# Kernel optimization log

Hardware: AMD Instinct MI355X
Metric: run time of the kernel (lower is better)

Reference implementation:

```python
import jax, jax.numpy as jnp
import numpy as np

N = 100_000   # nodes
E = 3_200_000 # edges (avg degree 32)
IN, HID, OUT = 1433, 16, 7  # hardcoded in Method_GCN_Class.__init__


def setup_inputs() -> dict:
    key = jax.random.key(0)
    ks = jax.random.split(key, 6)
    x = jax.random.normal(ks[0], (N, IN), dtype=jnp.float32)
    adj_row = jax.random.randint(ks[1], (E,), 0, N, dtype=jnp.int32)
    adj_col = jax.random.randint(ks[2], (E,), 0, N, dtype=jnp.int32)
    adj_val = jax.random.uniform(ks[3], (E,), dtype=jnp.float32)
    W1 = jax.random.uniform(ks[4], (IN, HID), dtype=jnp.float32)  # nn.init.uniform_
    b1 = jnp.zeros((HID,), dtype=jnp.float32)
    W2 = jax.random.uniform(ks[5], (HID, OUT), dtype=jnp.float32)
    b2 = jnp.zeros((OUT,), dtype=jnp.float32)
    return dict(x=x, adj_row=adj_row, adj_col=adj_col, adj_val=adj_val,
                W1=W1, b1=b1, W2=W2, b2=b2)


def _spmm(row, col, val, dense):
    # torch.sparse.mm(adj, dense) with adj in COO form: out[r] += val*dense[c]
    return jax.ops.segment_sum(val[:, None] * dense[col], row, num_segments=N)


def reference(x, adj_row, adj_col, adj_val, W1, b1, W2, b2):
    # layer 1: graph_conv -> relu (dropout p=0.1 is a no-op at inference)
    h = _spmm(adj_row, adj_col, adj_val, x @ W1) + b1
    h = jax.nn.relu(h)
    # layer 2: graph_conv -> log_softmax over classes
    h = _spmm(adj_row, adj_col, adj_val, h @ W2) + b2
    return jax.nn.log_softmax(h, axis=1)
```

## Files before the change

kernel.cpp:

```cpp
#include <hip/hip_runtime.h>
#include <math.h>

#define IN_F 1433
#define HID  16
#define OUTC 7
#define SCAN_T 1024

#define K1_THREADS 512
#define K1_ROWS_W  8
#define K1_ROWS_B  64
#define KA         768
#define LDSW       17
#define K1_LDS_FLOATS (KA * LDSW)

#define RPB      128
#define BCAP     4480
#define PCH      2048
#define OVF_CAP  131072

typedef float f4_t __attribute__((ext_vector_type(4)));
typedef f4_t uf4 __attribute__((aligned(4)));

__host__ __device__ __forceinline__ int imin(int a, int b) { return a < b ? a : b; }

__global__ __launch_bounds__(256) void zero_i32(int4* __restrict__ p, int n4)
{
    int i = blockIdx.x * blockDim.x + threadIdx.x;
    if (i < n4) p[i] = make_int4(0, 0, 0, 0);
}

__device__ __forceinline__ void k1_body(
    const float* __restrict__ x, const float* __restrict__ W1,
    float* __restrict__ XW, int N, int vbid, float* sW)
{
    const int wave = threadIdx.x >> 6;
    const int lane = threadIdx.x & 63;
    const int ks   = lane & 15;
    const int j4   = lane >> 4;
    const int row0 = vbid * K1_ROWS_B + wave * K1_ROWS_W;

    int xoff[K1_ROWS_W];
#pragma unroll
    for (int r = 0; r < K1_ROWS_W; ++r) {
        int row = row0 + r;
        if (row > N - 1) row = N - 1;
        if (row < 0) row = 0;
        xoff[r] = row * IN_F;
    }

    float acc[K1_ROWS_W][4];
#pragma unroll
    for (int r = 0; r < K1_ROWS_W; ++r)
#pragma unroll
        for (int jj = 0; jj < 4; ++jj) acc[r][jj] = 0.f;

#pragma unroll 1
    for (int p = 0; p < 2; ++p) {
        const int pbase = p ? KA : 0;
        const int pk    = p ? (IN_F - KA) : KA;
        if (p) __syncthreads();
        for (int f = threadIdx.x; f < pk * HID; f += K1_THREADS)
            sW[(f >> 4) * LDSW + (f & 15)] = W1[pbase * HID + f];
        __syncthreads();

        const int nfull = pk >> 6;
#pragma unroll 1
        for (int c = 0; c < nfull; ++c) {
            const int kb = c * 64 + ks * 4;
            uf4 xq[K1_ROWS_W];
#pragma unroll
            for (int r = 0; r < K1_ROWS_W; ++r)
                xq[r] = *(const uf4*)(x + (size_t)xoff[r] + pbase + kb);
            float w[4][4];
#pragma unroll
            for (int kk = 0; kk < 4; ++kk) {
                const float* wr = sW + (size_t)(kb + kk) * LDSW + j4 * 4;
                w[kk][0] = wr[0]; w[kk][1] = wr[1];
                w[kk][2] = wr[2]; w[kk][3] = wr[3];
            }
#pragma unroll
            for (int kk = 0; kk < 4; ++kk)
#pragma unroll
                for (int r = 0; r < K1_ROWS_W; ++r) {
                    const float xv = xq[r][kk];
                    acc[r][0] += xv * w[kk][0];
                    acc[r][1] += xv * w[kk][1];
                    acc[r][2] += xv * w[kk][2];
                    acc[r][3] += xv * w[kk][3];
                }
        }

        const int tb = nfull * 64 + ks * 4;
        if (tb < pk + 3 && (pk & 63)) {
#pragma unroll
            for (int kk = 0; kk < 4; ++kk) {
                const int kloc = tb + kk;
                const bool ok = (kloc < pk);
                const float* wr = sW + (size_t)kloc * LDSW + j4 * 4;
                float w0 = wr[0], w1 = wr[1], w2 = wr[2], w3 = wr[3];
#pragma unroll
                for (int r = 0; r < K1_ROWS_W; ++r) {
                    const float xv = ok ? x[(size_t)xoff[r] + pbase + kloc] : 0.f;
                    acc[r][0] += xv * w0;
                    acc[r][1] += xv * w1;
                    acc[r][2] += xv * w2;
                    acc[r][3] += xv * w3;
                }
            }
        }
    }

#pragma unroll
    for (int m = 1; m <= 8; m <<= 1)
#pragma unroll
        for (int r = 0; r < K1_ROWS_W; ++r)
#pragma unroll
            for (int jj = 0; jj < 4; ++jj)
                acc[r][jj] += __shfl_xor(acc[r][jj], m);

    if (ks == 0) {
#pragma unroll
        for (int r = 0; r < K1_ROWS_W; ++r) {
            const int row = row0 + r;
            if (row >= 0 && row < N) {
                float4 o = make_float4(acc[r][0], acc[r][1], acc[r][2], acc[r][3]);
                *(float4*)(XW + (size_t)row * HID + j4 * 4) = o;
            }
        }
    }
}

__device__ __forceinline__ void partition_body(
    const int* __restrict__ arow, const int* __restrict__ acol,
    const float* __restrict__ aval, int* __restrict__ cursor,
    int2* __restrict__ buckets, int* __restrict__ ovf, int* __restrict__ ovfc,
    int E, int nbuk, int sb, int nsb, int* hist)
{
    const int nch = (E + PCH - 1) / PCH;
    for (int ch = sb; ch < nch; ch += nsb) {
        const int e0 = ch * PCH;
        const int e1 = imin(e0 + PCH, E);
        for (int b = threadIdx.x; b < nbuk; b += K1_THREADS) hist[b] = 0;
        __syncthreads();

        int rr[4], cc[4]; float vv[4];
        int nl = 0;
        const int base = e0 + threadIdx.x * 4;
        if (base + 3 < e1) {
            int4 r4 = *(const int4*)(arow + base);
            int4 c4 = *(const int4*)(acol + base);
            float4 v4 = *(const float4*)(aval + base);
            rr[0]=r4.x; rr[1]=r4.y; rr[2]=r4.z; rr[3]=r4.w;
            cc[0]=c4.x; cc[1]=c4.y; cc[2]=c4.z; cc[3]=c4.w;
            vv[0]=v4.x; vv[1]=v4.y; vv[2]=v4.z; vv[3]=v4.w;
            nl = 4;
        } else {
            for (int i = base; i < e1 && nl < 4; ++i) {
                rr[nl] = arow[i]; cc[nl] = acol[i]; vv[nl] = aval[i];
                ++nl;
            }
        }
        for (int u = 0; u < nl; ++u) atomicAdd(&hist[rr[u] >> 7], 1);
        __syncthreads();

        for (int b = threadIdx.x; b < nbuk; b += K1_THREADS) {
            const int h = hist[b];
            hist[b] = (h > 0) ? atomicAdd(&cursor[b], h) : 0;
        }
        __syncthreads();

        for (int u = 0; u < nl; ++u) {
            const int b = rr[u] >> 7;
            const int pos = atomicAdd(&hist[b], 1);
            if (pos < BCAP) {
                buckets[(size_t)b * BCAP + pos] =
                    make_int2(((rr[u] & (RPB - 1)) << 17) | cc[u],
                              __float_as_int(vv[u]));
            } else {
                int op = atomicAdd(ovfc, 1);
                if (op < OVF_CAP) {
                    ovf[3 * op]     = rr[u];
                    ovf[3 * op + 1] = cc[u];
                    ovf[3 * op + 2] = __float_as_int(vv[u]);
                }
            }
        }
        __syncthreads();
    }
}

__global__ __launch_bounds__(K1_THREADS) void k1_partition(
    const float* __restrict__ x, const float* __restrict__ W1,
    float* __restrict__ XW, int N, int k1b,
    const int* __restrict__ arow, const int* __restrict__ acol,
    const float* __restrict__ aval, int* __restrict__ cursor,
    int2* __restrict__ buckets, int* __restrict__ ovf, int* __restrict__ ovfc,
    int E, int nbuk, int scb)
{
    __shared__ float sW[K1_LDS_FLOATS];
    const int bid = blockIdx.x;
    if ((bid % 4 == 3) && (bid / 4 < scb)) {
        partition_body(arow, acol, aval, cursor, buckets, ovf, ovfc,
                       E, nbuk, bid / 4, scb, (int*)sW);
        return;
    }
    const int k1_idx = bid - imin((bid + 1) / 4, scb);
    if (k1_idx >= k1b) return;
    k1_body(x, W1, XW, N, k1_idx, sW);
}

__global__ __launch_bounds__(512) void bucket_repack(
    const int* __restrict__ cursor, int2* __restrict__ buckets,
    int* __restrict__ rowptrB, int* __restrict__ ovf, int* __restrict__ ovfc,
    int nbuk)
{
    __shared__ int2 ebuf[BCAP];
    __shared__ int rcnt[RPB];
    __shared__ int rcur[RPB];
    __shared__ int rbase[RPB + 1];
    const int b = blockIdx.x;
    const int cnt_b = imin(cursor[b], BCAP);
    int2* src = buckets + (size_t)b * BCAP;

    for (int r = threadIdx.x; r < RPB; r += 512) { rcnt[r] = 0; rcur[r] = 0; }
    __syncthreads();

    for (int i = threadIdx.x; i < cnt_b; i += 512)
        atomicAdd(&rcnt[src[i].x >> 17], 1);
    __syncthreads();

    if (threadIdx.x == 0) {
        int run = 0;
        for (int r = 0; r < RPB; ++r) {
            rbase[r] = run;
            run += (rcnt[r] + 1) & ~1;
        }
        rbase[RPB] = run;
    }
    __syncthreads();

    for (int r = threadIdx.x; r < RPB; r += 512) {
        if (rcnt[r] & 1) {
            const int pp = rbase[r] + rcnt[r];
            if (pp < BCAP) ebuf[pp] = make_int2(0, 0);
        }
    }
    __syncthreads();

    for (int i = threadIdx.x; i < cnt_b; i += 512) {
        const int2 ed = src[i];
        const int rl = ed.x >> 17;
        const int pos = rbase[rl] + atomicAdd(&rcur[rl], 1);
        if (pos < BCAP) {
            ebuf[pos] = make_int2(ed.x & 0x1FFFF, ed.y);
        } else {
            int op = atomicAdd(ovfc, 1);
            if (op < OVF_CAP) {
                ovf[3 * op]     = b * RPB + rl;
                ovf[3 * op + 1] = ed.x & 0x1FFFF;
                ovf[3 * op + 2] = ed.y;
            }
        }
    }
    __syncthreads();

    const int total = imin(rbase[RPB], BCAP);
    for (int i = threadIdx.x; i < total; i += 512) src[i] = ebuf[i];
    for (int r = threadIdx.x; r < RPB; r += 512)
        rowptrB[b * (RPB + 1) + r] = imin(rbase[r], BCAP);
    if (threadIdx.x == 0)
        rowptrB[b * (RPB + 1) + RPB] = total;
}

__global__ __launch_bounds__(256) void ovf_apply16(
    const int* __restrict__ ovf, const int* __restrict__ ovfc,
    const float* __restrict__ XW, float* __restrict__ Hx)
{
    const int n = imin(ovfc[0], OVF_CAP);
    const int tid = blockIdx.x * blockDim.x + threadIdx.x;
    const int stride = gridDim.x * blockDim.x;
    for (int i = tid; i < n; i += stride) {
        const int r = ovf[3 * i], c = ovf[3 * i + 1];
        const float v = __int_as_float(ovf[3 * i + 2]);
        const float* src = XW + (size_t)c * HID;
        float* dst = Hx + (size_t)r * HID;
#pragma unroll
        for (int j = 0; j < HID; ++j) atomicAdd(dst + j, v * src[j]);
    }
}

__global__ __launch_bounds__(256) void ovf_apply7(
    const int* __restrict__ ovf, const int* __restrict__ ovfc,
    const float* __restrict__ h2, float* __restrict__ Ox)
{
    const int n = imin(ovfc[0], OVF_CAP);
    const int tid = blockIdx.x * blockDim.x + threadIdx.x;
    const int stride = gridDim.x * blockDim.x;
    for (int i = tid; i < n; i += stride) {
        const int r = ovf[3 * i], c = ovf[3 * i + 1];
        const float v = __int_as_float(ovf[3 * i + 2]);
        const float* src = h2 + (size_t)c * 8;
        float* dst = Ox + (size_t)r * 8;
#pragma unroll
        for (int j = 0; j < OUTC; ++j) atomicAdd(dst + j, v * src[j]);
    }
}

__global__ __launch_bounds__(256) void spmm16B(
    const int* __restrict__ rowptrB, const int2* __restrict__ buckets,
    const float* __restrict__ XW, const float* __restrict__ Hx,
    const float* __restrict__ b1, const float* __restrict__ W2,
    float* __restrict__ h2, int N)
{
    const int gw = (int)((blockIdx.x * (size_t)blockDim.x + threadIdx.x) >> 6);
    if (gw >= N) return;
    const int lane = threadIdx.x & 63;
    const int j = lane & 15;
    const int w = lane >> 4;
    const int b  = gw >> 7;
    const int rl = gw & (RPB - 1);
    const int rs = rowptrB[b * (RPB + 1) + rl];
    const int re = rowptrB[b * (RPB + 1) + rl + 1];
    const int2* base = buckets + (size_t)b * BCAP;

    float acc = 0.f;
    int k = rs + w * 4;
    while (k + 4 <= re) {
        const int4* q = (const int4*)(base + k);
        int4 A = q[0], B = q[1];
        acc += __int_as_float(A.y) * XW[(size_t)A.x * HID + j];
        acc += __int_as_float(A.w) * XW[(size_t)A.z * HID + j];
        acc += __int_as_float(B.y) * XW[(size_t)B.x * HID + j];
        acc += __int_as_float(B.w) * XW[(size_t)B.z * HID + j];
        k += 16;
    }
    for (; k < re; ++k) {
        int2 a = base[k];
        acc += __int_as_float(a.y) * XW[(size_t)a.x * HID + j];
    }
    acc += __shfl_xor(acc, 16);
    acc += __shfl_xor(acc, 32);
    acc += Hx[(size_t)gw * HID + j];

    const float h = fmaxf(acc + b1[j], 0.f);
    float p[OUTC];
#pragma unroll
    for (int c = 0; c < OUTC; ++c) p[c] = h * W2[j * OUTC + c];
#pragma unroll
    for (int m = 1; m <= 8; m <<= 1)
#pragma unroll
        for (int c = 0; c < OUTC; ++c) p[c] += __shfl_xor(p[c], m);

    if (lane < 8) {
        float o = p[0];
        o = (lane == 1) ? p[1] : o;
        o = (lane == 2) ? p[2] : o;
        o = (lane == 3) ? p[3] : o;
        o = (lane == 4) ? p[4] : o;
        o = (lane == 5) ? p[5] : o;
        o = (lane == 6) ? p[6] : o;
        if (lane == 7) o = 0.f;
        h2[(size_t)gw * 8 + lane] = o;
    }
}

__global__ __launch_bounds__(256) void spmm7B(
    const int* __restrict__ rowptrB, const int2* __restrict__ buckets,
    const float* __restrict__ h2, const float* __restrict__ Ox,
    const float* __restrict__ b2, float* __restrict__ out, int N)
{
    const int gw = (int)((blockIdx.x * (size_t)blockDim.x + threadIdx.x) >> 6);
    if (gw >= N) return;
    const int lane = threadIdx.x & 63;
    const int j = lane & 7;
    const int w = lane >> 3;
    const int b  = gw >> 7;
    const int rl = gw & (RPB - 1);
    const int rs = rowptrB[b * (RPB + 1) + rl];
    const int re = rowptrB[b * (RPB + 1) + rl + 1];
    const int2* base = buckets + (size_t)b * BCAP;

    float acc = 0.f;
    int k = rs + w * 4;
    while (k + 4 <= re) {
        const int4* q = (const int4*)(base + k);
        int4 A = q[0], B = q[1];
        acc += __int_as_float(A.y) * h2[(size_t)A.x * 8 + j];
        acc += __int_as_float(A.w) * h2[(size_t)A.z * 8 + j];
        acc += __int_as_float(B.y) * h2[(size_t)B.x * 8 + j];
        acc += __int_as_float(B.w) * h2[(size_t)B.z * 8 + j];
        k += 32;
    }
    for (; k < re; ++k) {
        int2 a = base[k];
        acc += __int_as_float(a.y) * h2[(size_t)a.x * 8 + j];
    }
    acc += __shfl_xor(acc, 8);
    acc += __shfl_xor(acc, 16);
    acc += __shfl_xor(acc, 32);
    acc += Ox[(size_t)gw * 8 + j];

    const float bias = b2[(j < OUTC) ? j : 0];
    const float val  = acc + bias;
    float mx = (j < OUTC) ? val : -INFINITY;
    mx = fmaxf(mx, __shfl_xor(mx, 1));
    mx = fmaxf(mx, __shfl_xor(mx, 2));
    mx = fmaxf(mx, __shfl_xor(mx, 4));
    float ex = (j < OUTC) ? expf(val - mx) : 0.f;
    ex += __shfl_xor(ex, 1);
    ex += __shfl_xor(ex, 2);
    ex += __shfl_xor(ex, 4);
    if (lane < OUTC) out[(size_t)gw * OUTC + lane] = val - mx - logf(ex);
}

__device__ __forceinline__ void hist_body(
    const int* __restrict__ arow, int* __restrict__ cnt, int E, int hb, int nhb)
{
    const int tid = hb * K1_THREADS + threadIdx.x;
    const int stride = nhb * K1_THREADS;
    const int E4 = E >> 2;
    const int4* a4 = (const int4*)arow;
    for (int v = tid; v < E4; v += stride) {
        int4 r = a4[v];
        atomicAdd(&cnt[r.x], 1);
        atomicAdd(&cnt[r.y], 1);
        atomicAdd(&cnt[r.z], 1);
        atomicAdd(&cnt[r.w], 1);
    }
    for (int v = E4 * 4 + tid; v < E; v += stride) atomicAdd(&cnt[arow[v]], 1);
}

__device__ __forceinline__ void scatter_body(
    const int* __restrict__ arow, const int* __restrict__ acol,
    const float* __restrict__ aval, int* __restrict__ cursor,
    int2* __restrict__ ecv, int E, int sb, int nsb)
{
    const int tid = sb * K1_THREADS + threadIdx.x;
    const int stride = nsb * K1_THREADS;
    const int E4 = E >> 2;
    const int4*   ar4 = (const int4*)arow;
    const int4*   ac4 = (const int4*)acol;
    const float4* av4 = (const float4*)aval;
    for (int v = tid; v < E4; v += stride) {
        int4 r = ar4[v];
        int4 c = ac4[v];
        float4 val = av4[v];
        int p0 = atomicAdd(&cursor[r.x], 1);
        int p1 = atomicAdd(&cursor[r.y], 1);
        int p2 = atomicAdd(&cursor[r.z], 1);
        int p3 = atomicAdd(&cursor[r.w], 1);
        ecv[p0] = make_int2(c.x, __float_as_int(val.x));
        ecv[p1] = make_int2(c.y, __float_as_int(val.y));
        ecv[p2] = make_int2(c.z, __float_as_int(val.z));
        ecv[p3] = make_int2(c.w, __float_as_int(val.w));
    }
    for (int v = E4 * 4 + tid; v < E; v += stride) {
        int pos = atomicAdd(&cursor[arow[v]], 1);
        ecv[pos] = make_int2(acol[v], __float_as_int(aval[v]));
    }
}

__global__ __launch_bounds__(K1_THREADS) void k1_hist_fused(
    const float* __restrict__ x, const float* __restrict__ W1,
    float* __restrict__ XW, int N, int half1,
    const int* __restrict__ arow, int* __restrict__ cnt, int E, int histB)
{
    __shared__ float sW[K1_LDS_FLOATS];
    const int bid = blockIdx.x;
    if ((bid % 3 == 2) && (bid / 3 < histB)) {
        hist_body(arow, cnt, E, bid / 3, histB);
        return;
    }
    const int k1_idx = bid - imin((bid + 1) / 3, histB);
    if (k1_idx >= half1) return;
    k1_body(x, W1, XW, N, k1_idx, sW);
}

__global__ __launch_bounds__(K1_THREADS) void k1_scatter_fused(
    const float* __restrict__ x, const float* __restrict__ W1,
    float* __restrict__ XW, int N, int half1, int half2,
    const int* __restrict__ arow, const int* __restrict__ acol,
    const float* __restrict__ aval, int* __restrict__ cursor,
    int2* __restrict__ ecv, int E, int scb)
{
    __shared__ float sW[K1_LDS_FLOATS];
    const int bid = blockIdx.x;
    if ((bid % 3 == 2) && (bid / 3 < scb)) {
        scatter_body(arow, acol, aval, cursor, ecv, E, bid / 3, scb);
        return;
    }
    const int k1_idx = bid - imin((bid + 1) / 3, scb) + half1;
    if (k1_idx >= half1 + half2) return;
    k1_body(x, W1, XW, N, k1_idx, sW);
}

__global__ __launch_bounds__(K1_THREADS) void gcn_k1_xw(
    const float* __restrict__ x, const float* __restrict__ W1,
    float* __restrict__ XW, int N)
{
    __shared__ float sW[K1_LDS_FLOATS];
    k1_body(x, W1, XW, N, blockIdx.x, sW);
}

__global__ __launch_bounds__(256) void csr_hist(
    const int* __restrict__ arow, int* __restrict__ cnt, int E)
{
    int e = blockIdx.x * blockDim.x + threadIdx.x;
    if (e < E) atomicAdd(&cnt[arow[e]], 1);
}

__global__ __launch_bounds__(256) void csr_scatter(
    const int* __restrict__ arow, const int* __restrict__ acol,
    const float* __restrict__ aval, int* __restrict__ cursor,
    int2* __restrict__ ecv, int E)
{
    int e = blockIdx.x * blockDim.x + threadIdx.x;
    if (e >= E) return;
    int pos = atomicAdd(&cursor[arow[e]], 1);
    ecv[pos] = make_int2(acol[e], __float_as_int(aval[e]));
}

__global__ __launch_bounds__(SCAN_T) void csr_scan(
    const int* __restrict__ cnt, int* __restrict__ rowptr,
    int* __restrict__ cursor, int N)
{
    __shared__ int sums[SCAN_T];
    const int t = threadIdx.x;
    const int chunk = (((N + SCAN_T - 1) / SCAN_T) + 3) & ~3;
    const int lo = t * chunk;
    int s = 0;
    const bool full = (lo + chunk <= N);
    if (full) {
        const int4* c4 = (const int4*)(cnt + lo);
#pragma unroll 4
        for (int i = 0; i < chunk / 4; ++i) {
            int4 v = c4[i];
            s += ((v.x + 1) & ~1) + ((v.y + 1) & ~1)
               + ((v.z + 1) & ~1) + ((v.w + 1) & ~1);
        }
    } else {
        const int hi = (lo + chunk < N) ? lo + chunk : N;
        for (int i = lo; i < hi; ++i) s += (cnt[i] + 1) & ~1;
    }
    sums[t] = s;
    __syncthreads();
    for (int d = 1; d < SCAN_T; d <<= 1) {
        int a = sums[t];
        int b = (t >= d) ? sums[t - d] : 0;
        __syncthreads();
        sums[t] = a + b;
        __syncthreads();
    }
    int run = sums[t] - s;
    if (full) {
        const int4* c4 = (const int4*)(cnt + lo);
        int4* rp4 = (int4*)(rowptr + lo);
        int4* cu4 = (int4*)(cursor + lo);
        for (int i = 0; i < chunk / 4; ++i) {
            int4 v = c4[i];
            int4 o;
            o.x = run; run += (v.x + 1) & ~1;
            o.y = run; run += (v.y + 1) & ~1;
            o.z = run; run += (v.z + 1) & ~1;
            o.w = run; run += (v.w + 1) & ~1;
            rp4[i] = o;
            cu4[i] = o;
        }
    } else {
        const int hi = (lo + chunk < N) ? lo + chunk : N;
        for (int i = lo; i < hi; ++i) {
            rowptr[i] = run;
            cursor[i] = run;
            run += (cnt[i] + 1) & ~1;
        }
    }
    if (t == SCAN_T - 1) rowptr[N] = sums[SCAN_T - 1];
}

__global__ __launch_bounds__(256) void spmm16_h2(
    const int* __restrict__ rowptr, const int2* __restrict__ ecv,
    const float* __restrict__ XW, const float* __restrict__ b1,
    const float* __restrict__ W2, float* __restrict__ h2, int N)
{
    const int gw = (int)((blockIdx.x * (size_t)blockDim.x + threadIdx.x) >> 6);
    if (gw >= N) return;
    const int lane = threadIdx.x & 63;
    const int j = lane & 15;
    const int w = lane >> 4;
    const int s = rowptr[gw], e = rowptr[gw + 1];

    float acc = 0.f;
    int k = s + w * 4;
    while (k + 4 <= e) {
        const int4* q = (const int4*)(ecv + k);
        int4 A = q[0], B = q[1];
        acc += __int_as_float(A.y) * XW[(size_t)A.x * HID + j];
        acc += __int_as_float(A.w) * XW[(size_t)A.z * HID + j];
        acc += __int_as_float(B.y) * XW[(size_t)B.x * HID + j];
        acc += __int_as_float(B.w) * XW[(size_t)B.z * HID + j];
        k += 16;
    }
    for (; k < e; ++k) {
        int2 a = ecv[k];
        acc += __int_as_float(a.y) * XW[(size_t)a.x * HID + j];
    }
    acc += __shfl_xor(acc, 16);
    acc += __shfl_xor(acc, 32);

    const float h = fmaxf(acc + b1[j], 0.f);
    float p[OUTC];
#pragma unroll
    for (int c = 0; c < OUTC; ++c) p[c] = h * W2[j * OUTC + c];
#pragma unroll
    for (int m = 1; m <= 8; m <<= 1)
#pragma unroll
        for (int c = 0; c < OUTC; ++c) p[c] += __shfl_xor(p[c], m);

    if (lane < 8) {
        float o = p[0];
        o = (lane == 1) ? p[1] : o;
        o = (lane == 2) ? p[2] : o;
        o = (lane == 3) ? p[3] : o;
        o = (lane == 4) ? p[4] : o;
        o = (lane == 5) ? p[5] : o;
        o = (lane == 6) ? p[6] : o;
        if (lane == 7) o = 0.f;
        h2[(size_t)gw * 8 + lane] = o;
    }
}

__global__ __launch_bounds__(256) void spmm7_lsm(
    const int* __restrict__ rowptr, const int2* __restrict__ ecv,
    const float* __restrict__ h2, const float* __restrict__ b2,
    float* __restrict__ out, int N)
{
    const int gw = (int)((blockIdx.x * (size_t)blockDim.x + threadIdx.x) >> 6);
    if (gw >= N) return;
    const int lane = threadIdx.x & 63;
    const int j = lane & 7;
    const int w = lane >> 3;
    const int s = rowptr[gw], e = rowptr[gw + 1];

    float acc = 0.f;
    int k = s + w * 4;
    while (k + 4 <= e) {
        const int4* q = (const int4*)(ecv + k);
        int4 A = q[0], B = q[1];
        acc += __int_as_float(A.y) * h2[(size_t)A.x * 8 + j];
        acc += __int_as_float(A.w) * h2[(size_t)A.z * 8 + j];
        acc += __int_as_float(B.y) * h2[(size_t)B.x * 8 + j];
        acc += __int_as_float(B.w) * h2[(size_t)B.z * 8 + j];
        k += 32;
    }
    for (; k < e; ++k) {
        int2 a = ecv[k];
        acc += __int_as_float(a.y) * h2[(size_t)a.x * 8 + j];
    }
    acc += __shfl_xor(acc, 8);
    acc += __shfl_xor(acc, 16);
    acc += __shfl_xor(acc, 32);

    const float bias = b2[(j < OUTC) ? j : 0];
    const float val  = acc + bias;
    float mx = (j < OUTC) ? val : -INFINITY;
    mx = fmaxf(mx, __shfl_xor(mx, 1));
    mx = fmaxf(mx, __shfl_xor(mx, 2));
    mx = fmaxf(mx, __shfl_xor(mx, 4));
    float ex = (j < OUTC) ? expf(val - mx) : 0.f;
    ex += __shfl_xor(ex, 1);
    ex += __shfl_xor(ex, 2);
    ex += __shfl_xor(ex, 4);
    if (lane < OUTC) out[(size_t)gw * OUTC + lane] = val - mx - logf(ex);
}

__global__ __launch_bounds__(256) void gcn_k2_spmm16_atomic(
    const int* __restrict__ arow, const int* __restrict__ acol,
    const float* __restrict__ aval, const float* __restrict__ XW,
    float* __restrict__ H, int E)
{
    int e = blockIdx.x * blockDim.x + threadIdx.x;
    if (e >= E) return;
    const int r = arow[e], c = acol[e];
    const float v = aval[e];
    const float4* src = (const float4*)(XW + (size_t)c * HID);
    float4 a = src[0], b = src[1], cc = src[2], d = src[3];
    float* dst = H + (size_t)r * HID;
    atomicAdd(dst + 0,  v * a.x);  atomicAdd(dst + 1,  v * a.y);
    atomicAdd(dst + 2,  v * a.z);  atomicAdd(dst + 3,  v * a.w);
    atomicAdd(dst + 4,  v * b.x);  atomicAdd(dst + 5,  v * b.y);
    atomicAdd(dst + 6,  v * b.z);  atomicAdd(dst + 7,  v * b.w);
    atomicAdd(dst + 8,  v * cc.x); atomicAdd(dst + 9,  v * cc.y);
    atomicAdd(dst + 10, v * cc.z); atomicAdd(dst + 11, v * cc.w);
    atomicAdd(dst + 12, v * d.x);  atomicAdd(dst + 13, v * d.y);
    atomicAdd(dst + 14, v * d.z);  atomicAdd(dst + 15, v * d.w);
}

__global__ __launch_bounds__(256) void gcn_k3_h2(
    const float* __restrict__ H, const float* __restrict__ b1,
    const float* __restrict__ W2, float* __restrict__ h2, int N)
{
    __shared__ float sW2[HID * OUTC];
    __shared__ float sb1[HID];
    if (threadIdx.x < HID * OUTC) sW2[threadIdx.x] = W2[threadIdx.x];
    if (threadIdx.x < HID)        sb1[threadIdx.x] = b1[threadIdx.x];
    __syncthreads();

    int row = blockIdx.x * blockDim.x + threadIdx.x;
    if (row >= N) return;

    const float4* hp = (const float4*)(H + (size_t)row * HID);
    float4 h0 = hp[0], h1 = hp[1], h2v = hp[2], h3 = hp[3];
    float h[16] = {h0.x, h0.y, h0.z, h0.w, h1.x, h1.y, h1.z, h1.w,
                   h2v.x, h2v.y, h2v.z, h2v.w, h3.x, h3.y, h3.z, h3.w};
#pragma unroll
    for (int i = 0; i < HID; ++i) {
        h[i] += sb1[i];
        h[i] = h[i] > 0.f ? h[i] : 0.f;
    }
    float o[8];
#pragma unroll
    for (int jj = 0; jj < OUTC; ++jj) {
        float sum = 0.f;
#pragma unroll
        for (int i = 0; i < HID; ++i) sum += h[i] * sW2[i * OUTC + jj];
        o[jj] = sum;
    }
    o[7] = 0.f;
    float4* op = (float4*)(h2 + (size_t)row * 8);
    op[0] = make_float4(o[0], o[1], o[2], o[3]);
    op[1] = make_float4(o[4], o[5], o[6], o[7]);
}

__global__ __launch_bounds__(256) void gcn_k4_spmm7_atomic(
    const int* __restrict__ arow, const int* __restrict__ acol,
    const float* __restrict__ aval, const float* __restrict__ h2,
    float* __restrict__ out, int E)
{
    int e = blockIdx.x * blockDim.x + threadIdx.x;
    if (e >= E) return;
    const int r = arow[e], c = acol[e];
    const float v = aval[e];
    const float* src = h2 + (size_t)c * 8;
    float* dst = out + (size_t)r * OUTC;
#pragma unroll
    for (int jj = 0; jj < OUTC; ++jj) atomicAdd(dst + jj, v * src[jj]);
}

__global__ __launch_bounds__(256) void gcn_k5_lsm(
    float* __restrict__ out, const float* __restrict__ b2, int N)
{
    int row = blockIdx.x * blockDim.x + threadIdx.x;
    if (row >= N) return;
    float* p = out + (size_t)row * OUTC;
    float v[OUTC];
#pragma unroll
    for (int jj = 0; jj < OUTC; ++jj) v[jj] = p[jj] + b2[jj];
    float m = v[0];
#pragma unroll
    for (int jj = 1; jj < OUTC; ++jj) m = fmaxf(m, v[jj]);
    float s = 0.f;
#pragma unroll
    for (int jj = 0; jj < OUTC; ++jj) s += expf(v[jj] - m);
    const float ls = logf(s);
#pragma unroll
    for (int jj = 0; jj < OUTC; ++jj) p[jj] = v[jj] - m - ls;
}

extern "C" void kernel_launch(void* const* d_in, const int* in_sizes, int n_in,
                              void* d_out, int out_size, void* d_ws, size_t ws_size,
                              hipStream_t stream)
{
    const float* x    = (const float*)d_in[0];
    const int*   arow = (const int*)d_in[1];
    const int*   acol = (const int*)d_in[2];
    const float* aval = (const float*)d_in[3];
    const float* W1   = (const float*)d_in[4];
    const float* b1   = (const float*)d_in[5];
    const float* W2   = (const float*)d_in[6];
    const float* b2   = (const float*)d_in[7];
    float* out = (float*)d_out;

    const int N = in_sizes[0] / IN_F;
    const int E = in_sizes[1];

    const int Np4 = (N + 3) & ~3;
    const int eb  = (E + 255) / 256;
    const int nb  = (N + 255) / 256;
    const int k1b = (N + K1_ROWS_B - 1) / K1_ROWS_B;
    const int nbuk = (N + RPB - 1) / RPB;
    const int scb1 = imin(384, k1b / 4);

    {
        char* wsp = (char*)d_ws;
        int2*  buckets = (int2*)wsp;  wsp += (size_t)nbuk * BCAP * 8;
        float* XW      = (float*)wsp; wsp += (size_t)N * HID * 4;
        float* h2      = (float*)wsp; wsp += (size_t)N * 8 * 4;
        int*   ovf     = (int*)wsp;   wsp += (size_t)OVF_CAP * 12;
        int*   rowptrB = (int*)wsp;   wsp += (size_t)nbuk * (RPB + 1) * 4;
        char*  zbase   = wsp;
        int*   cursor  = (int*)wsp;   wsp += (size_t)((nbuk + 3) & ~3) * 4;
        float* Hx      = (float*)wsp; wsp += (size_t)N * HID * 4;
        float* Ox      = (float*)wsp; wsp += (size_t)N * 8 * 4;
        int*   ovfc    = (int*)wsp;   wsp += 16;
        const size_t need1 = (size_t)(wsp - (char*)d_ws);

        if (ws_size >= need1 && scb1 >= 1 && N <= (1 << 17) &&
            nbuk <= K1_LDS_FLOATS) {
            const size_t zbytes = (size_t)(wsp - zbase);
            const int n4z = (int)(zbytes / 16);
            zero_i32<<<(n4z + 255) / 256, 256, 0, stream>>>((int4*)zbase, n4z);

            k1_partition<<<k1b + scb1, K1_THREADS, 0, stream>>>(
                x, W1, XW, N, k1b, arow, acol, aval, cursor, buckets,
                ovf, ovfc, E, nbuk, scb1);
            bucket_repack<<<nbuk, 512, 0, stream>>>(
                cursor, buckets, rowptrB, ovf, ovfc, nbuk);
            ovf_apply16<<<128, 256, 0, stream>>>(ovf, ovfc, XW, Hx);
            spmm16B<<<(N + 3) / 4, 256, 0, stream>>>(
                rowptrB, buckets, XW, Hx, b1, W2, h2, N);
            ovf_apply7<<<128, 256, 0, stream>>>(ovf, ovfc, h2, Ox);
            spmm7B<<<(N + 3) / 4, 256, 0, stream>>>(
                rowptrB, buckets, h2, Ox, b2, out, N);
            return;
        }
    }

    {
        const int EPAD = E + N + 8;
        char* wsp = (char*)d_ws;
        int2*  ecv    = (int2*)wsp;   wsp += (size_t)EPAD * 8;
        int*   cnt    = (int*)wsp;    wsp += (size_t)Np4 * 4;
        int*   cursor = (int*)wsp;    wsp += (size_t)Np4 * 4;
        int*   rowptr = (int*)wsp;    wsp += (size_t)(Np4 + 4) * 4;
        float* XW     = (float*)wsp;  wsp += (size_t)N * HID * 4;
        float* h2     = (float*)wsp;  wsp += (size_t)N * 8 * 4;
        const size_t need2 = (size_t)(wsp - (char*)d_ws);

        if (ws_size >= need2) {
            const size_t zbytes = (size_t)EPAD * 8 + (size_t)Np4 * 4;
            const int n4z = (int)((zbytes + 15) / 16);
            zero_i32<<<(n4z + 255) / 256, 256, 0, stream>>>((int4*)d_ws, n4z);

            const int half1 = (k1b + 1) / 2;
            const int half2 = k1b - half1;
            const int histB = imin(384, half1 / 2);
            const int scb   = imin(384, half2 / 2);

            if (histB >= 1 && scb >= 1) {
                k1_hist_fused<<<half1 + histB, K1_THREADS, 0, stream>>>(
                    x, W1, XW, N, half1, arow, cnt, E, histB);
                csr_scan<<<1, SCAN_T, 0, stream>>>(cnt, rowptr, cursor, N);
                k1_scatter_fused<<<half2 + scb, K1_THREADS, 0, stream>>>(
                    x, W1, XW, N, half1, half2, arow, acol, aval, cursor, ecv, E, scb);
            } else {
                csr_hist<<<eb, 256, 0, stream>>>(arow, cnt, E);
                csr_scan<<<1, SCAN_T, 0, stream>>>(cnt, rowptr, cursor, N);
                csr_scatter<<<eb, 256, 0, stream>>>(arow, acol, aval, cursor, ecv, E);
                gcn_k1_xw<<<k1b, K1_THREADS, 0, stream>>>(x, W1, XW, N);
            }

            spmm16_h2<<<(N + 3) / 4, 256, 0, stream>>>(rowptr, ecv, XW, b1, W2, h2, N);
            spmm7_lsm<<<(N + 3) / 4, 256, 0, stream>>>(rowptr, ecv, h2, b2, out, N);
            return;
        }
    }

    {
        float* XWf = (float*)d_ws;
        float* Hf  = XWf + (size_t)N * HID;
        float* h2f = XWf;
        const int hz4 = (int)(((size_t)N * HID) / 4);
        zero_i32<<<(hz4 + 255) / 256, 256, 0, stream>>>((int4*)Hf, hz4);
        (void)hipMemsetAsync(out, 0, (size_t)N * OUTC * sizeof(float), stream);
        gcn_k1_xw<<<k1b, K1_THREADS, 0, stream>>>(x, W1, XWf, N);
        gcn_k2_spmm16_atomic<<<eb, 256, 0, stream>>>(arow, acol, aval, XWf, Hf, E);
        gcn_k3_h2<<<nb, 256, 0, stream>>>(Hf, b1, W2, h2f, N);
        gcn_k4_spmm7_atomic<<<eb, 256, 0, stream>>>(arow, acol, aval, h2f, out, E);
        gcn_k5_lsm<<<nb, 256, 0, stream>>>(out, b2, N);
    }
}
```

Before: 378.4 us.

## Shrink K1 LDS chunk and switch to scalar x loads for higher occupancy

```diff
diff --git a/kernel.cpp b/kernel.cpp
--- a/kernel.cpp
+++ b/kernel.cpp
@@ -9,17 +9,14 @@
 #define K1_THREADS 512
 #define K1_ROWS_W  8
 #define K1_ROWS_B  64
-#define KA         768
+#define KCH        560
 #define LDSW       17
-#define K1_LDS_FLOATS (KA * LDSW)
+#define K1_LDS_FLOATS (KCH * LDSW)
 
 #define RPB      128
 #define BCAP     4480
 #define PCH      2048
 #define OVF_CAP  131072
-
-typedef float f4_t __attribute__((ext_vector_type(4)));
-typedef f4_t uf4 __attribute__((aligned(4)));
 
 __host__ __device__ __forceinline__ int imin(int a, int b) { return a < b ? a : b; }
 
@@ -55,57 +52,48 @@
         for (int jj = 0; jj < 4; ++jj) acc[r][jj] = 0.f;
 
 #pragma unroll 1
-    for (int p = 0; p < 2; ++p) {
-        const int pbase = p ? KA : 0;
-        const int pk    = p ? (IN_F - KA) : KA;
+    for (int p = 0; p < 3; ++p) {
+        const int pbase = p * KCH;
+        const int pk    = imin(KCH, IN_F - pbase);
         if (p) __syncthreads();
         for (int f = threadIdx.x; f < pk * HID; f += K1_THREADS)
             sW[(f >> 4) * LDSW + (f & 15)] = W1[pbase * HID + f];
         __syncthreads();
 
-        const int nfull = pk >> 6;
-#pragma unroll 1
+        const int nfull = pk >> 4;
+#pragma unroll 2
         for (int c = 0; c < nfull; ++c) {
-            const int kb = c * 64 + ks * 4;
-            uf4 xq[K1_ROWS_W];
+            const int kloc = c * 16 + ks;
+            const float* wr = sW + (size_t)kloc * LDSW + j4 * 4;
+            float w0 = wr[0], w1 = wr[1], w2 = wr[2], w3 = wr[3];
+            float xv[K1_ROWS_W];
 #pragma unroll
             for (int r = 0; r < K1_ROWS_W; ++r)
-                xq[r] = *(const uf4*)(x + (size_t)xoff[r] + pbase + kb);
-            float w[4][4];
-#pragma unroll
-            for (int kk = 0; kk < 4; ++kk) {
-                const float* wr = sW + (size_t)(kb + kk) * LDSW + j4 * 4;
-                w[kk][0] = wr[0]; w[kk][1] = wr[1];
-                w[kk][2] = wr[2]; w[kk][3] = wr[3];
+                xv[r] = x[(size_t)xoff[r] + pbase + kloc];
+#pragma unroll
+            for (int r = 0; r < K1_ROWS_W; ++r) {
+                acc[r][0] += xv[r] * w0;
+                acc[r][1] += xv[r] * w1;
+                acc[r][2] += xv[r] * w2;
+                acc[r][3] += xv[r] * w3;
             }
-#pragma unroll
-            for (int kk = 0; kk < 4; ++kk)
-#pragma unroll
-                for (int r = 0; r < K1_ROWS_W; ++r) {
-                    const float xv = xq[r][kk];
-                    acc[r][0] += xv * w[kk][0];
-                    acc[r][1] += xv * w[kk][1];
-                    acc[r][2] += xv * w[kk][2];
-                    acc[r][3] += xv * w[kk][3];
-                }
-        }
-
-        const int tb = nfull * 64 + ks * 4;
-        if (tb < pk + 3 && (pk & 63)) {
-#pragma unroll
-            for (int kk = 0; kk < 4; ++kk) {
-                const int kloc = tb + kk;
-                const bool ok = (kloc < pk);
-                const float* wr = sW + (size_t)kloc * LDSW + j4 * 4;
-                float w0 = wr[0], w1 = wr[1], w2 = wr[2], w3 = wr[3];
-#pragma unroll
-                for (int r = 0; r < K1_ROWS_W; ++r) {
-                    const float xv = ok ? x[(size_t)xoff[r] + pbase + kloc] : 0.f;
-                    acc[r][0] += xv * w0;
-                    acc[r][1] += xv * w1;
-                    acc[r][2] += xv * w2;
-                    acc[r][3] += xv * w3;
-                }
+        }
+
+        if (pk & 15) {
+            const int kloc = nfull * 16 + ks;
+            const bool ok = (kloc < pk);
+            const float* wr = sW + (size_t)kloc * LDSW + j4 * 4;
+            float w0 = wr[0], w1 = wr[1], w2 = wr[2], w3 = wr[3];
+            float xv[K1_ROWS_W];
+#pragma unroll
+            for (int r = 0; r < K1_ROWS_W; ++r)
+                xv[r] = ok ? x[(size_t)xoff[r] + pbase + kloc] : 0.f;
+#pragma unroll
+            for (int r = 0; r < K1_ROWS_W; ++r) {
+                acc[r][0] += xv[r] * w0;
+                acc[r][1] += xv[r] * w1;
+                acc[r][2] += xv[r] * w2;
+                acc[r][3] += xv[r] * w3;
             }
         }
     }
@@ -189,7 +177,7 @@
     }
 }
 
-__global__ __launch_bounds__(K1_THREADS) void k1_partition(
+__global__ __launch_bounds__(K1_THREADS, 8) void k1_partition(
     const float* __restrict__ x, const float* __restrict__ W1,
     float* __restrict__ XW, int N, int k1b,
     const int* __restrict__ arow, const int* __restrict__ acol,
@@ -460,7 +448,7 @@
     }
 }
 
-__global__ __launch_bounds__(K1_THREADS) void k1_hist_fused(
+__global__ __launch_bounds__(K1_THREADS, 8) void k1_hist_fused(
     const float* __restrict__ x, const float* __restrict__ W1,
     float* __restrict__ XW, int N, int half1,
     const int* __restrict__ arow, int* __restrict__ cnt, int E, int histB)
@@ -476,7 +464,7 @@
     k1_body(x, W1, XW, N, k1_idx, sW);
 }
 
-__global__ __launch_bounds__(K1_THREADS) void k1_scatter_fused(
+__global__ __launch_bounds__(K1_THREADS, 8) void k1_scatter_fused(
     const float* __restrict__ x, const float* __restrict__ W1,
     float* __restrict__ XW, int N, int half1, int half2,
     const int* __restrict__ arow, const int* __restrict__ acol,
@@ -494,7 +482,7 @@
     k1_body(x, W1, XW, N, k1_idx, sW);
 }
 
-__global__ __launch_bounds__(K1_THREADS) void gcn_k1_xw(
+__global__ __launch_bounds__(K1_THREADS, 8) void gcn_k1_xw(
     const float* __restrict__ x, const float* __restrict__ W1,
     float* __restrict__ XW, int N)
 {
```

New measurement: 1.273 ms. 236% more time.
